# Kernel optimization log

Hardware: AMD Instinct MI355X
Metric: run time of the kernel (lower is better)

## Reference

```python
import jax, jax.numpy as jnp
import numpy as np

G, N, E = 64, 1000, 8192          # graphs, nodes/graph, edges/graph
F_IN, C, H, HID, NCLS = 128, 128, 4, 256, 2
EPS = 1e-5


def _gcn(x, src, dst, W, b):
    # GCNConv: symmetric normalization with self-loops, sum aggregation.
    h = x @ W                                              # [N, C]
    deg = jax.ops.segment_sum(jnp.ones(E, h.dtype), dst, num_segments=N) + 1.0
    dinv = jax.lax.rsqrt(deg)                              # deg^{-1/2}
    msg = h[src] * (dinv[src] * dinv[dst])[:, None]        # [E, C] gather
    out = jax.ops.segment_sum(msg, dst, num_segments=N)    # scatter-add
    out = out + h * (dinv * dinv)[:, None]                 # self-loop term
    return out + b


def _layernorm(y, g, b):
    mu = y.mean(-1, keepdims=True)
    var = ((y - mu) ** 2).mean(-1, keepdims=True)
    return (y - mu) * jax.lax.rsqrt(var + EPS) * g + b


def setup_inputs() -> dict:
    key = jax.random.key(0)
    ks = jax.random.split(key, 12)
    rn = lambda k, s: jax.random.normal(k, s, jnp.float32) * 0.05
    return dict(
        x=jax.random.normal(ks[0], (G, N, F_IN), jnp.float32),
        edge_index=jax.random.randint(ks[1], (G, 2, E), 0, N),
        W0=rn(ks[2], (F_IN, C)), b0=jnp.zeros((C,), jnp.float32),
        W1=rn(ks[3], (C, C)), b1=jnp.zeros((C,), jnp.float32),
        in_w=rn(ks[4], (3 * C, C)), in_b=jnp.zeros((3 * C,), jnp.float32),
        out_w=rn(ks[5], (C, C)), out_b=jnp.zeros((C,), jnp.float32),
        ln2_g=jnp.ones((C,), jnp.float32), ln2_b=jnp.zeros((C,), jnp.float32),
        mw1=rn(ks[6], (C, HID)), mb1=jnp.zeros((HID,), jnp.float32),
        mw2=rn(ks[7], (HID, C)), mb2=jnp.zeros((C,), jnp.float32),
        lw=rn(ks[8], (C, NCLS)), lb=jnp.zeros((NCLS,), jnp.float32),
    )


def reference(x, edge_index, W0, b0, W1, b1, in_w, in_b, out_w, out_b,
              ln2_g, ln2_b, mw1, mb1, mw2, mb2, lw, lb):
    src, dst = edge_index[:, 0, :], edge_index[:, 1, :]
    conv = jax.vmap(_gcn, in_axes=(0, 0, 0, None, None))
    h = jnp.tanh(conv(x, src, dst, W0, b0))   # [G, N, C]
    h = jnp.tanh(conv(h, src, dst, W1, b1))
    g = h.sum(axis=1)                          # SumAggregation -> [G, C]

    # MultiheadAttention, unbatched: sequence of G graph embeddings
    qkv = g @ in_w.T + in_b
    q, k, v = jnp.split(qkv, 3, axis=-1)
    d = C // H
    qh, kh, vh = (t.reshape(G, H, d) for t in (q, k, v))
    attn = jax.nn.softmax(jnp.einsum('qhd,khd->hqk', qh, kh) * (d ** -0.5), axis=-1)
    o = jnp.einsum('hqk,khd->qhd', attn, vh).reshape(G, C) @ out_w.T + out_b

    x_attend = o                               # dropout = identity (eval)
    # NOTE: original computes layer_norm1(x_attend) but immediately overwrites it.
    mlp = jnp.maximum(x_attend @ mw1 + mb1, 0.0) @ mw2 + mb2
    y = _layernorm(x_attend + mlp, ln2_g, ln2_b)
    node_repr = jnp.maximum(y, 0.0).sum(axis=0)  # [C]
    return node_repr @ lw + lb                   # [NCLS]
```

## Files before the change

### kernel.cpp

```cpp
#include <hip/hip_runtime.h>
#include <math.h>

#define Gn 64
#define Nn 1000
#define En 8192
#define Cc 128
#define HIDn 256
#define EPSf 1e-5f

typedef __attribute__((ext_vector_type(8))) short bh8;
typedef __attribute__((ext_vector_type(4))) float fx4;

__device__ __forceinline__ unsigned short f2bf(float f) {
    unsigned u = __float_as_uint(f);
    u += 0x7fffu + ((u >> 16) & 1u);
    return (unsigned short)(u >> 16);
}
__device__ __forceinline__ float bflo(unsigned u) { return __uint_as_float(u << 16); }
__device__ __forceinline__ float bfhi(unsigned u) { return __uint_as_float(u & 0xffff0000u); }

__global__ __launch_bounds__(256) void k_wt(const float* __restrict__ W0, const float* __restrict__ W1,
                                            unsigned short* __restrict__ Wt0g,
                                            unsigned short* __restrict__ Wt1g)
{
    __shared__ __align__(16) short Wls[128][136];
    int t = threadIdx.x;
    const float* Wsrc = (blockIdx.x == 0) ? W0 : W1;
    unsigned short* Wdst = (blockIdx.x == 0) ? Wt0g : Wt1g;
    for (int idx = t; idx < 16384; idx += 256) {
        int kI = idx >> 7, n = idx & 127;
        Wls[n][kI] = (short)f2bf(Wsrc[idx]);
    }
    __syncthreads();
    for (int idx = t; idx < 2048; idx += 256) {
        int n = idx >> 4, kc = idx & 15;
        *(bh8*)(Wdst + (size_t)idx * 8) = *(const bh8*)&Wls[n][kc * 8];
    }
}

__global__ __launch_bounds__(512) void k_front(const int* __restrict__ ei, const float* __restrict__ X,
                                               const unsigned short* __restrict__ Wt0g,
                                               int4* __restrict__ ninfo, int2* __restrict__ epair,
                                               float* __restrict__ pooled, float* __restrict__ repr,
                                               int* __restrict__ bars,
                                               unsigned short* __restrict__ Hout)
{
    __shared__ __align__(16) short Wt[128][136];
    __shared__ int wsum[8];
    int t = threadIdx.x;
    int b = blockIdx.x;

    if (b < 64) {
        int* curs = (int*)&Wt[0][0];
        float* dinv_s = (float*)((char*)&Wt[0][0] + 4096);
        int g = b;
        const int* srcp = ei + (size_t)g * 2 * En;
        const int* dstp = srcp + En;
        int lane = t & 63, wv = t >> 6;

        curs[t * 2] = 0; curs[t * 2 + 1] = 0;
        __syncthreads();
        for (int e = t; e < En; e += 512) atomicAdd(&curs[dstp[e]], 1);
        __syncthreads();

        int base = t * 2;
        int d0 = curs[base], d1 = curs[base + 1];
        int s = d0 + d1;
        int v = s;
        #pragma unroll
        for (int off = 1; off <= 32; off <<= 1) {
            int u = __shfl_up(v, off);
            if (lane >= off) v += u;
        }
        if (lane == 63) wsum[wv] = v;
        __syncthreads();
        int woff = 0;
        #pragma unroll
        for (int w = 0; w < 8; ++w) if (w < wv) woff += wsum[w];
        int e0 = woff + v - s;
        int e1 = e0 + d0;
        float dv0 = rsqrtf((float)d0 + 1.f), dv1 = rsqrtf((float)d1 + 1.f);
        curs[base] = e0; curs[base + 1] = e1;
        dinv_s[base] = dv0; dinv_s[base + 1] = dv1;
        if (base < Nn)     ninfo[g * Nn + base]     = make_int4(e0, d0, __float_as_int(dv0 * dv0), 0);
        if (base + 1 < Nn) ninfo[g * Nn + base + 1] = make_int4(e1, d1, __float_as_int(dv1 * dv1), 0);
        __syncthreads();

        for (int e = t; e < En; e += 512) {
            int dd = dstp[e], ss = srcp[e];
            int p = atomicAdd(&curs[dd], 1);
            float w = dinv_s[ss] * dinv_s[dd];
            epair[(size_t)g * En + p] = make_int2(ss, __float_as_int(w));
        }
        if (t < Cc) pooled[g * Cc + t] = 0.f;
        if (g == 0 && t < Cc) repr[t] = 0.f;
        if (g == 0 && t < 4) bars[t] = 0;
        return;
    }

    int bb = b - 64;
    int xcd = bb & 7, gg = (bb >> 3) & 7, rblk = bb >> 6;
    int g = xcd + 8 * gg;
    for (int idx = t; idx < 2048; idx += 512) {
        int n = idx >> 4, kc = idx & 15;
        *(bh8*)&Wt[n][kc * 8] = *(const bh8*)(Wt0g + (size_t)idx * 8);
    }
    __syncthreads();

    int wave = t >> 6, l = t & 63;
    int lr = l & 15, lg = l >> 4;
    const float* Xf = X + (size_t)g * Nn * Cc;
    unsigned short* Hg = Hout + (size_t)g * Nn * Cc;

    int rbase = rblk * 128 + wave * 16;
    int r = rbase + lr;
    bool ok = r < Nn;
    bh8 af[4];
    #pragma unroll
    for (int ks = 0; ks < 4; ++ks) {
        if (ok) {
            const float* xp = Xf + (size_t)r * Cc + ks * 32 + lg * 8;
            fx4 a0 = *(const fx4*)xp;
            fx4 a1 = *(const fx4*)(xp + 4);
            bh8 av;
            av[0] = (short)f2bf(a0[0]); av[1] = (short)f2bf(a0[1]);
            av[2] = (short)f2bf(a0[2]); av[3] = (short)f2bf(a0[3]);
            av[4] = (short)f2bf(a1[0]); av[5] = (short)f2bf(a1[1]);
            av[6] = (short)f2bf(a1[2]); av[7] = (short)f2bf(a1[3]);
            af[ks] = av;
        } else af[ks] = bh8{0, 0, 0, 0, 0, 0, 0, 0};
    }
    fx4 acc[8];
    #pragma unroll
    for (int ct = 0; ct < 8; ++ct) acc[ct] = fx4{0.f, 0.f, 0.f, 0.f};
    #pragma unroll
    for (int ks = 0; ks < 4; ++ks) {
        #pragma unroll
        for (int ct = 0; ct < 8; ++ct) {
            bh8 bfr = *(const bh8*)(&Wt[ct * 16 + lr][ks * 32 + lg * 8]);
            acc[ct] = __builtin_amdgcn_mfma_f32_16x16x32_bf16(af[ks], bfr, acc[ct], 0, 0, 0);
        }
    }
    #pragma unroll
    for (int ct = 0; ct < 8; ++ct) {
        #pragma unroll
        for (int rg = 0; rg < 4; ++rg) {
            int row = rbase + lg * 4 + rg;
            if (row < Nn) Hg[(size_t)row * Cc + ct * 16 + lr] = f2bf(acc[ct][rg]);
        }
    }
}

__global__ __launch_bounds__(256) void k_gemm1(const unsigned short* __restrict__ Xh,
                                               const unsigned short* __restrict__ Wtg,
                                               unsigned short* __restrict__ Hout)
{
    __shared__ __align__(16) short Wt[128][136];
    int b = blockIdx.x;
    int xcd = b & 7, gg = (b >> 3) & 7, rblk = b >> 6;
    int g = xcd + 8 * gg;
    int t = threadIdx.x;
    for (int idx = t; idx < 2048; idx += 256) {
        int n = idx >> 4, kc = idx & 15;
        bh8 v = *(const bh8*)(Wtg + (size_t)idx * 8);
        *(bh8*)&Wt[n][kc * 8] = v;
    }
    __syncthreads();

    int wave = t >> 6, l = t & 63;
    int lr = l & 15, lg = l >> 4;
    const short* Xg = (const short*)Xh + (size_t)g * Nn * Cc;
    unsigned short* Hg = Hout + (size_t)g * Nn * Cc;

    int rbase = rblk * 64 + wave * 16;
    int r = rbase + lr;
    bool ok = r < Nn;
    bh8 af[4];
    #pragma unroll
    for (int ks = 0; ks < 4; ++ks) {
        if (ok) af[ks] = *(const bh8*)(Xg + (size_t)r * Cc + ks * 32 + lg * 8);
        else    af[ks] = bh8{0, 0, 0, 0, 0, 0, 0, 0};
    }
    fx4 acc[8];
    #pragma unroll
    for (int ct = 0; ct < 8; ++ct) acc[ct] = fx4{0.f, 0.f, 0.f, 0.f};
    #pragma unroll
    for (int ks = 0; ks < 4; ++ks) {
        #pragma unroll
        for (int ct = 0; ct < 8; ++ct) {
            bh8 bfr = *(const bh8*)(&Wt[ct * 16 + lr][ks * 32 + lg * 8]);
            acc[ct] = __builtin_amdgcn_mfma_f32_16x16x32_bf16(af[ks], bfr, acc[ct], 0, 0, 0);
        }
    }
    #pragma unroll
    for (int ct = 0; ct < 8; ++ct) {
        #pragma unroll
        for (int rg = 0; rg < 4; ++rg) {
            int row = rbase + lg * 4 + rg;
            if (row < Nn) Hg[(size_t)row * Cc + ct * 16 + lr] = f2bf(acc[ct][rg]);
        }
    }
}

template<int POOL>
__global__ __launch_bounds__(256) void k_combine(const unsigned* __restrict__ Hb, const int2* __restrict__ epair,
                                                 const int4* __restrict__ ninfo, const float* __restrict__ bias,
                                                 unsigned* __restrict__ Tout, float* __restrict__ pooled)
{
    int b = blockIdx.x;
    int xcd = b & 7, j = b >> 3;
    int g = xcd + 8 * (j & 7);
    int blk = j >> 3;
    int wave = threadIdx.x >> 6, lane = threadIdx.x & 63;
    const unsigned* Hg = Hb + (size_t)g * Nn * 64;
    const int2* epg = epair + (size_t)g * En;
    const int4* nig = ninfo + (size_t)g * Nn;
    float2 bb = *(const float2*)(bias + lane * 2);
    float px = 0.f, py = 0.f;
    for (int n = blk * 4 + wave; n < Nn; n += 128) {
        int4 ni = nig[n];
        int st = ni.x, dc = ni.y;
        float sw = __int_as_float(ni.z);
        unsigned hv = Hg[(size_t)n * 64 + lane];
        float a0x = bflo(hv) * sw + bb.x, a0y = bfhi(hv) * sw + bb.y;
        float a1x = 0.f, a1y = 0.f, a2x = 0.f, a2y = 0.f, a3x = 0.f, a3y = 0.f;
        int e = 0;
        for (; e + 4 <= dc; e += 4) {
            int2 p0 = epg[st + e];
            int2 p1 = epg[st + e + 1];
            int2 p2 = epg[st + e + 2];
            int2 p3 = epg[st + e + 3];
            unsigned r0 = Hg[(size_t)p0.x * 64 + lane];
            unsigned r1 = Hg[(size_t)p1.x * 64 + lane];
            unsigned r2 = Hg[(size_t)p2.x * 64 + lane];
            unsigned r3 = Hg[(size_t)p3.x * 64 + lane];
            float w0 = __int_as_float(p0.y), w1 = __int_as_float(p1.y);
            float w2 = __int_as_float(p2.y), w3 = __int_as_float(p3.y);
            a0x = fmaf(bflo(r0), w0, a0x); a0y = fmaf(bfhi(r0), w0, a0y);
            a1x = fmaf(bflo(r1), w1, a1x); a1y = fmaf(bfhi(r1), w1, a1y);
            a2x = fmaf(bflo(r2), w2, a2x); a2y = fmaf(bfhi(r2), w2, a2y);
            a3x = fmaf(bflo(r3), w3, a3x); a3y = fmaf(bfhi(r3), w3, a3y);
        }
        for (; e < dc; ++e) {
            int2 p0 = epg[st + e];
            unsigned r0 = Hg[(size_t)p0.x * 64 + lane];
            float w0 = __int_as_float(p0.y);
            a0x = fmaf(bflo(r0), w0, a0x); a0y = fmaf(bfhi(r0), w0, a0y);
        }
        float ax = (a0x + a1x) + (a2x + a3x);
        float ay = (a0y + a1y) + (a2y + a3y);
        float tx = tanhf(ax), ty = tanhf(ay);
        if (POOL) { px += tx; py += ty; }
        else Tout[(size_t)(g * Nn + n) * 64 + lane] = ((unsigned)f2bf(ty) << 16) | (unsigned)f2bf(tx);
    }
    if (POOL) {
        atomicAdd(&pooled[g * Cc + lane * 2], px);
        atomicAdd(&pooled[g * Cc + lane * 2 + 1], py);
    }
}

__global__ __launch_bounds__(1024) void k_qkv(const float* __restrict__ pooled, const float* __restrict__ in_w,
                                              const float* __restrict__ in_b, float* __restrict__ qkvb)
{
    int t = threadIdx.x, lane = t & 63, wv = t >> 6;
    int c = blockIdx.x * 16 + wv;
    const float* wr = in_w + c * Cc;
    float w0 = wr[lane], w1 = wr[64 + lane];
    float bias = in_b[c];
    for (int i = 0; i < Gn; ++i) {
        float p = fmaf(pooled[i * Cc + lane], w0, pooled[i * Cc + 64 + lane] * w1);
        #pragma unroll
        for (int off2 = 32; off2 > 0; off2 >>= 1) p += __shfl_xor(p, off2);
        if (lane == 0) qkvb[i * 384 + c] = p + bias;
    }
}

__global__ __launch_bounds__(1024) void k_attn(const float* __restrict__ qkvb, float* __restrict__ ob)
{
    __shared__ float q[64][33], kk[64][33], v[64][33];
    __shared__ float S[64][64];
    int h = blockIdx.x, t = threadIdx.x;

    for (int idx = t; idx < 2048; idx += 1024) {
        int i = idx >> 5, cc = idx & 31;
        q[i][cc]  = qkvb[i * 384 + h * 32 + cc];
        kk[i][cc] = qkvb[i * 384 + 128 + h * 32 + cc];
        v[i][cc]  = qkvb[i * 384 + 256 + h * 32 + cc];
    }
    __syncthreads();

    for (int idx = t; idx < 4096; idx += 1024) {
        int i = idx >> 6, jj = idx & 63;
        float acc = 0.f;
        #pragma unroll
        for (int d2 = 0; d2 < 32; ++d2) acc = fmaf(q[i][d2], kk[jj][d2], acc);
        S[i][jj] = acc * 0.17677669529663687f;
    }
    __syncthreads();

    int lane = t & 63, w = t >> 6;
    for (int r = w; r < 64; r += 16) {
        float val = S[r][lane];
        float m = val;
        #pragma unroll
        for (int off = 32; off > 0; off >>= 1) m = fmaxf(m, __shfl_xor(m, off));
        float e2 = expf(val - m);
        float ssum = e2;
        #pragma unroll
        for (int off = 32; off > 0; off >>= 1) ssum += __shfl_xor(ssum, off);
        S[r][lane] = e2 / ssum;
    }
    __syncthreads();

    for (int idx = t; idx < 2048; idx += 1024) {
        int i = idx >> 5, d2 = idx & 31;
        float acc = 0.f;
        #pragma unroll 4
        for (int k2 = 0; k2 < 64; ++k2) acc = fmaf(S[i][k2], v[k2][d2], acc);
        ob[i * Cc + h * 32 + d2] = acc;
    }
}

__global__ __launch_bounds__(512) void k_tailfinal(const float* __restrict__ ob, const float* __restrict__ out_w,
                                                   const float* __restrict__ out_b, const float* __restrict__ mw1,
                                                   const float* __restrict__ mb1, const float* __restrict__ mw2,
                                                   const float* __restrict__ mb2, const float* __restrict__ ln2g,
                                                   const float* __restrict__ ln2b, const float* __restrict__ lw,
                                                   const float* __restrict__ lb, float* __restrict__ repr,
                                                   int* __restrict__ ctr, float* __restrict__ out)
{
    __shared__ float sob[128];
    __shared__ float sxatt[128];
    __shared__ float sm1p[2][256];
    __shared__ float sm1[256];
    __shared__ float sp2[4][128];
    __shared__ float yb[128];
    __shared__ int slast;
    int g = blockIdx.x;
    int t = threadIdx.x, lane = t & 63, wv = t >> 6;

    if (t < 128) sob[t] = ob[(size_t)g * Cc + t];
    __syncthreads();

    {
        float o0 = sob[lane], o1 = sob[64 + lane];
        for (int c = wv; c < Cc; c += 8) {
            const float* wr = out_w + c * Cc;
            float p = fmaf(o0, wr[lane], o1 * wr[64 + lane]);
            #pragma unroll
            for (int off = 32; off > 0; off >>= 1) p += __shfl_xor(p, off);
            if (lane == 0) sxatt[c] = p + out_b[c];
        }
    }
    __syncthreads();

    {
        int jc = t & 255, half = t >> 8;
        int k0b = half * 64;
        float a[8];
        #pragma unroll
        for (int u = 0; u < 8; ++u) a[u] = 0.f;
        for (int k0 = k0b; k0 < k0b + 64; k0 += 8) {
            #pragma unroll
            for (int u = 0; u < 8; ++u)
                a[u] = fmaf(sxatt[k0 + u], mw1[(size_t)(k0 + u) * HIDn + jc], a[u]);
        }
        sm1p[half][jc] = ((a[0] + a[1]) + (a[2] + a[3])) + ((a[4] + a[5]) + (a[6] + a[7]));
        __syncthreads();
        if (t < 256) sm1[t] = fmaxf(sm1p[0][t] + sm1p[1][t] + mb1[t], 0.f);
    }
    __syncthreads();

    {
        int c = t & 127, q = t >> 7;
        int j0b = q * 64;
        float a[8];
        #pragma unroll
        for (int u = 0; u < 8; ++u) a[u] = 0.f;
        for (int j0 = j0b; j0 < j0b + 64; j0 += 8) {
            #pragma unroll
            for (int u = 0; u < 8; ++u)
                a[u] = fmaf(sm1[j0 + u], mw2[(size_t)(j0 + u) * Cc + c], a[u]);
        }
        sp2[q][c] = ((a[0] + a[1]) + (a[2] + a[3])) + ((a[4] + a[5]) + (a[6] + a[7]));
        __syncthreads();
        if (t < 128) yb[t] = sxatt[t] + (sp2[0][t] + sp2[1][t]) + (sp2[2][t] + sp2[3][t]) + mb2[t];
    }
    __syncthreads();

    if (t < 64) {
        float v0 = yb[lane], v1 = yb[64 + lane];
        float s = v0 + v1;
        #pragma unroll
        for (int off = 32; off > 0; off >>= 1) s += __shfl_xor(s, off);
        float mu = s * (1.f / 128.f);
        float d0 = v0 - mu, d1 = v1 - mu;
        float vv = d0 * d0 + d1 * d1;
        #pragma unroll
        for (int off = 32; off > 0; off >>= 1) vv += __shfl_xor(vv, off);
        float rstd = rsqrtf(vv * (1.f / 128.f) + EPSf);
        float z0 = fmaxf(d0 * rstd * ln2g[lane] + ln2b[lane], 0.f);
        float z1 = fmaxf(d1 * rstd * ln2g[64 + lane] + ln2b[64 + lane], 0.f);
        atomicAdd(&repr[lane], z0);
        atomicAdd(&repr[64 + lane], z1);
    }

    __threadfence();
    __syncthreads();
    if (t == 0) slast = atomicAdd(ctr, 1);
    __syncthreads();
    if (slast == 63) {
        __threadfence();
        __shared__ float r0s[128], r1s[128];
        if (t < 128) {
            float r = __hip_atomic_load(&repr[t], __ATOMIC_RELAXED, __HIP_MEMORY_SCOPE_AGENT);
            r0s[t] = r * lw[t * 2 + 0];
            r1s[t] = r * lw[t * 2 + 1];
        }
        __syncthreads();
        for (int s2 = 64; s2 > 0; s2 >>= 1) {
            if (t < s2) { r0s[t] += r0s[t + s2]; r1s[t] += r1s[t + s2]; }
            __syncthreads();
        }
        if (t == 0) { out[0] = r0s[0] + lb[0]; out[1] = r1s[0] + lb[1]; }
    }
}

extern "C" void kernel_launch(void* const* d_in, const int* in_sizes, int n_in,
                              void* d_out, int out_size, void* d_ws, size_t ws_size,
                              hipStream_t stream)
{
    const float* x     = (const float*)d_in[0];
    const int*   ei    = (const int*)d_in[1];
    const float* W0    = (const float*)d_in[2];
    const float* b0    = (const float*)d_in[3];
    const float* W1    = (const float*)d_in[4];
    const float* b1    = (const float*)d_in[5];
    const float* in_w  = (const float*)d_in[6];
    const float* in_b  = (const float*)d_in[7];
    const float* out_w = (const float*)d_in[8];
    const float* out_b = (const float*)d_in[9];
    const float* ln2g  = (const float*)d_in[10];
    const float* ln2b  = (const float*)d_in[11];
    const float* mw1   = (const float*)d_in[12];
    const float* mb1   = (const float*)d_in[13];
    const float* mw2   = (const float*)d_in[14];
    const float* mb2   = (const float*)d_in[15];
    const float* lw    = (const float*)d_in[16];
    const float* lb    = (const float*)d_in[17];
    float* out = (float*)d_out;
    (void)in_sizes; (void)n_in; (void)out_size; (void)ws_size;

    char* ws = (char*)d_ws;
    size_t off = 0;
    auto carve = [&](size_t bytes) { size_t o = off; off += (bytes + 255) & ~(size_t)255; return o; };
    size_t o_ni    = carve((size_t)Gn * Nn * 16);
    size_t o_ep    = carve((size_t)Gn * En * 8);
    size_t o_pool  = carve((size_t)Gn * Cc * 4);
    size_t o_qkv   = carve((size_t)Gn * 384 * 4);
    size_t o_ob    = carve((size_t)Gn * Cc * 4);
    size_t o_repr  = carve((size_t)Cc * 4);
    size_t o_bars  = carve(256);
    size_t o_W0t   = carve((size_t)Cc * Cc * 2);
    size_t o_W1t   = carve((size_t)Cc * Cc * 2);
    size_t o_H     = carve((size_t)Gn * Nn * Cc * 2);
    size_t o_T     = carve((size_t)Gn * Nn * Cc * 2);

    int4*  ninfo  = (int4*)(ws + o_ni);
    int2*  epair  = (int2*)(ws + o_ep);
    float* pooled = (float*)(ws + o_pool);
    float* qkvb   = (float*)(ws + o_qkv);
    float* ob     = (float*)(ws + o_ob);
    float* repr   = (float*)(ws + o_repr);
    int*   bars   = (int*)(ws + o_bars);
    unsigned short* Wt0g = (unsigned short*)(ws + o_W0t);
    unsigned short* Wt1g = (unsigned short*)(ws + o_W1t);
    unsigned short* H  = (unsigned short*)(ws + o_H);
    unsigned short* T  = (unsigned short*)(ws + o_T);

    k_wt<<<2, 256, 0, stream>>>(W0, W1, Wt0g, Wt1g);
    k_front<<<576, 512, 0, stream>>>(ei, x, Wt0g, ninfo, epair, pooled, repr, bars, H);
    k_combine<0><<<2048, 256, 0, stream>>>((const unsigned*)H, epair, ninfo, b0, (unsigned*)T, nullptr);
    k_gemm1<<<1024, 256, 0, stream>>>(T, Wt1g, H);
    k_combine<1><<<2048, 256, 0, stream>>>((const unsigned*)H, epair, ninfo, b1, nullptr, pooled);
    k_qkv<<<24, 1024, 0, stream>>>(pooled, in_w, in_b, qkvb);
    k_attn<<<4, 1024, 0, stream>>>(qkvb, ob);
    k_tailfinal<<<64, 512, 0, stream>>>(ob, out_w, out_b, mw1, mb1, mw2, mb2, ln2g, ln2b,
                                        lw, lb, repr, &bars[2], out);
}
```

Measured before the change: 160.1 us.

## Fuse attention into tail kernel, use fast tanh and pre-scaled gather offsets

Removes the separate 4-block attention kernel. Each tail block now recomputes its own query row's attention over all keys and values loaded into shared memory, which saves one launch and the round trip through the ob buffer. Separately, the combine kernels use an exp2/rcp based tanh instead of tanhf and store edge source indices pre-shifted to byte offsets, which removes multiply/size_t address arithmetic in the gather loop. The trade-off is that every tail block redundantly loads all 64 K/V rows (about 66KB of shared memory), and the fast tanh has slightly different accuracy.

Result: faster. 152.0 us (median of 2 runs) (-5.1%).

```diff
diff --git a/kernel.cpp b/kernel.cpp
--- a/kernel.cpp
+++ b/kernel.cpp
@@ -18,6 +18,10 @@
 }
 __device__ __forceinline__ float bflo(unsigned u) { return __uint_as_float(u << 16); }
 __device__ __forceinline__ float bfhi(unsigned u) { return __uint_as_float(u & 0xffff0000u); }
+__device__ __forceinline__ float tanh_fast(float x) {
+    float e = exp2f(x * 2.885390081777927f);
+    return 1.f - 2.f * __builtin_amdgcn_rcpf(e + 1.f);
+}
 
 __global__ __launch_bounds__(256) void k_wt(const float* __restrict__ W0, const float* __restrict__ W1,
                                             unsigned short* __restrict__ Wt0g,
@@ -90,7 +94,7 @@
             int dd = dstp[e], ss = srcp[e];
             int p = atomicAdd(&curs[dd], 1);
             float w = dinv_s[ss] * dinv_s[dd];
-            epair[(size_t)g * En + p] = make_int2(ss, __float_as_int(w));
+            epair[(size_t)g * En + p] = make_int2(ss << 8, __float_as_int(w));
         }
         if (t < Cc) pooled[g * Cc + t] = 0.f;
         if (g == 0 && t < Cc) repr[t] = 0.f;
@@ -212,16 +216,17 @@
     int g = xcd + 8 * (j & 7);
     int blk = j >> 3;
     int wave = threadIdx.x >> 6, lane = threadIdx.x & 63;
-    const unsigned* Hg = Hb + (size_t)g * Nn * 64;
+    const char* Hgc = (const char*)(Hb + (size_t)g * Nn * 64);
     const int2* epg = epair + (size_t)g * En;
     const int4* nig = ninfo + (size_t)g * Nn;
     float2 bb = *(const float2*)(bias + lane * 2);
+    int lb4 = lane * 4;
     float px = 0.f, py = 0.f;
     for (int n = blk * 4 + wave; n < Nn; n += 128) {
         int4 ni = nig[n];
         int st = ni.x, dc = ni.y;
         float sw = __int_as_float(ni.z);
-        unsigned hv = Hg[(size_t)n * 64 + lane];
+        unsigned hv = *(const unsigned*)(Hgc + n * 256 + lb4);
         float a0x = bflo(hv) * sw + bb.x, a0y = bfhi(hv) * sw + bb.y;
         float a1x = 0.f, a1y = 0.f, a2x = 0.f, a2y = 0.f, a3x = 0.f, a3y = 0.f;
         int e = 0;
@@ -230,10 +235,10 @@
             int2 p1 = epg[st + e + 1];
             int2 p2 = epg[st + e + 2];
             int2 p3 = epg[st + e + 3];
-            unsigned r0 = Hg[(size_t)p0.x * 64 + lane];
-            unsigned r1 = Hg[(size_t)p1.x * 64 + lane];
-            unsigned r2 = Hg[(size_t)p2.x * 64 + lane];
-            unsigned r3 = Hg[(size_t)p3.x * 64 + lane];
+            unsigned r0 = *(const unsigned*)(Hgc + p0.x + lb4);
+            unsigned r1 = *(const unsigned*)(Hgc + p1.x + lb4);
+            unsigned r2 = *(const unsigned*)(Hgc + p2.x + lb4);
+            unsigned r3 = *(const unsigned*)(Hgc + p3.x + lb4);
             float w0 = __int_as_float(p0.y), w1 = __int_as_float(p1.y);
             float w2 = __int_as_float(p2.y), w3 = __int_as_float(p3.y);
             a0x = fmaf(bflo(r0), w0, a0x); a0y = fmaf(bfhi(r0), w0, a0y);
@@ -243,13 +248,13 @@
         }
         for (; e < dc; ++e) {
             int2 p0 = epg[st + e];
-            unsigned r0 = Hg[(size_t)p0.x * 64 + lane];
+            unsigned r0 = *(const unsigned*)(Hgc + p0.x + lb4);
             float w0 = __int_as_float(p0.y);
             a0x = fmaf(bflo(r0), w0, a0x); a0y = fmaf(bfhi(r0), w0, a0y);
         }
         float ax = (a0x + a1x) + (a2x + a3x);
         float ay = (a0y + a1y) + (a2y + a3y);
-        float tx = tanhf(ax), ty = tanhf(ay);
+        float tx = tanh_fast(ax), ty = tanh_fast(ay);
         if (POOL) { px += tx; py += ty; }
         else Tout[(size_t)(g * Nn + n) * 64 + lane] = ((unsigned)f2bf(ty) << 16) | (unsigned)f2bf(tx);
     }
@@ -275,60 +280,18 @@
     }
 }
 
-__global__ __launch_bounds__(1024) void k_attn(const float* __restrict__ qkvb, float* __restrict__ ob)
-{
-    __shared__ float q[64][33], kk[64][33], v[64][33];
-    __shared__ float S[64][64];
-    int h = blockIdx.x, t = threadIdx.x;
-
-    for (int idx = t; idx < 2048; idx += 1024) {
-        int i = idx >> 5, cc = idx & 31;
-        q[i][cc]  = qkvb[i * 384 + h * 32 + cc];
-        kk[i][cc] = qkvb[i * 384 + 128 + h * 32 + cc];
-        v[i][cc]  = qkvb[i * 384 + 256 + h * 32 + cc];
-    }
-    __syncthreads();
-
-    for (int idx = t; idx < 4096; idx += 1024) {
-        int i = idx >> 6, jj = idx & 63;
-        float acc = 0.f;
-        #pragma unroll
-        for (int d2 = 0; d2 < 32; ++d2) acc = fmaf(q[i][d2], kk[jj][d2], acc);
-        S[i][jj] = acc * 0.17677669529663687f;
-    }
-    __syncthreads();
-
-    int lane = t & 63, w = t >> 6;
-    for (int r = w; r < 64; r += 16) {
-        float val = S[r][lane];
-        float m = val;
-        #pragma unroll
-        for (int off = 32; off > 0; off >>= 1) m = fmaxf(m, __shfl_xor(m, off));
-        float e2 = expf(val - m);
-        float ssum = e2;
-        #pragma unroll
-        for (int off = 32; off > 0; off >>= 1) ssum += __shfl_xor(ssum, off);
-        S[r][lane] = e2 / ssum;
-    }
-    __syncthreads();
-
-    for (int idx = t; idx < 2048; idx += 1024) {
-        int i = idx >> 5, d2 = idx & 31;
-        float acc = 0.f;
-        #pragma unroll 4
-        for (int k2 = 0; k2 < 64; ++k2) acc = fmaf(S[i][k2], v[k2][d2], acc);
-        ob[i * Cc + h * 32 + d2] = acc;
-    }
-}
-
-__global__ __launch_bounds__(512) void k_tailfinal(const float* __restrict__ ob, const float* __restrict__ out_w,
-                                                   const float* __restrict__ out_b, const float* __restrict__ mw1,
-                                                   const float* __restrict__ mb1, const float* __restrict__ mw2,
-                                                   const float* __restrict__ mb2, const float* __restrict__ ln2g,
-                                                   const float* __restrict__ ln2b, const float* __restrict__ lw,
-                                                   const float* __restrict__ lb, float* __restrict__ repr,
-                                                   int* __restrict__ ctr, float* __restrict__ out)
-{
+__global__ __launch_bounds__(512) void k_tail(const float* __restrict__ qkvb, const float* __restrict__ out_w,
+                                              const float* __restrict__ out_b, const float* __restrict__ mw1,
+                                              const float* __restrict__ mb1, const float* __restrict__ mw2,
+                                              const float* __restrict__ mb2, const float* __restrict__ ln2g,
+                                              const float* __restrict__ ln2b, const float* __restrict__ lw,
+                                              const float* __restrict__ lb, float* __restrict__ repr,
+                                              int* __restrict__ ctr, float* __restrict__ out)
+{
+    __shared__ float kk[64][129];
+    __shared__ float vv[64][129];
+    __shared__ float qrow[128];
+    __shared__ float S[4][64];
     __shared__ float sob[128];
     __shared__ float sxatt[128];
     __shared__ float sm1p[2][256];
@@ -339,7 +302,43 @@
     int g = blockIdx.x;
     int t = threadIdx.x, lane = t & 63, wv = t >> 6;
 
-    if (t < 128) sob[t] = ob[(size_t)g * Cc + t];
+    for (int idx = t; idx < 8192; idx += 512) {
+        int i = idx >> 7, c = idx & 127;
+        kk[i][c] = qkvb[i * 384 + 128 + c];
+        vv[i][c] = qkvb[i * 384 + 256 + c];
+    }
+    if (t < 128) qrow[t] = qkvb[g * 384 + t];
+    __syncthreads();
+
+    if (t < 256) {
+        int h = t >> 6, jj = t & 63;
+        int base = h * 32;
+        float acc = 0.f;
+        #pragma unroll
+        for (int d = 0; d < 32; ++d) acc = fmaf(qrow[base + d], kk[jj][base + d], acc);
+        S[h][jj] = acc * 0.17677669529663687f;
+    }
+    __syncthreads();
+    if (wv < 4) {
+        float val = S[wv][lane];
+        float m = val;
+        #pragma unroll
+        for (int off = 32; off > 0; off >>= 1) m = fmaxf(m, __shfl_xor(m, off));
+        float e2 = expf(val - m);
+        float ssum = e2;
+        #pragma unroll
+        for (int off = 32; off > 0; off >>= 1) ssum += __shfl_xor(ssum, off);
+        S[wv][lane] = e2 / ssum;
+    }
+    __syncthreads();
+    if (t < 128) {
+        int h = t >> 5, d = t & 31;
+        int col = h * 32 + d;
+        float acc = 0.f;
+        #pragma unroll 4
+        for (int j = 0; j < 64; ++j) acc = fmaf(S[h][j], vv[j][col], acc);
+        sob[col] = acc;
+    }
     __syncthreads();
 
     {
@@ -395,10 +394,10 @@
         for (int off = 32; off > 0; off >>= 1) s += __shfl_xor(s, off);
         float mu = s * (1.f / 128.f);
         float d0 = v0 - mu, d1 = v1 - mu;
-        float vv = d0 * d0 + d1 * d1;
-        #pragma unroll
-        for (int off = 32; off > 0; off >>= 1) vv += __shfl_xor(vv, off);
-        float rstd = rsqrtf(vv * (1.f / 128.f) + EPSf);
+        float vvr = d0 * d0 + d1 * d1;
+        #pragma unroll
+        for (int off = 32; off > 0; off >>= 1) vvr += __shfl_xor(vvr, off);
+        float rstd = rsqrtf(vvr * (1.f / 128.f) + EPSf);
         float z0 = fmaxf(d0 * rstd * ln2g[lane] + ln2b[lane], 0.f);
         float z1 = fmaxf(d1 * rstd * ln2g[64 + lane] + ln2b[64 + lane], 0.f);
         atomicAdd(&repr[lane], z0);
@@ -458,7 +457,6 @@
     size_t o_ep    = carve((size_t)Gn * En * 8);
     size_t o_pool  = carve((size_t)Gn * Cc * 4);
     size_t o_qkv   = carve((size_t)Gn * 384 * 4);
-    size_t o_ob    = carve((size_t)Gn * Cc * 4);
     size_t o_repr  = carve((size_t)Cc * 4);
     size_t o_bars  = carve(256);
     size_t o_W0t   = carve((size_t)Cc * Cc * 2);
@@ -470,7 +468,6 @@
     int2*  epair  = (int2*)(ws + o_ep);
     float* pooled = (float*)(ws + o_pool);
     float* qkvb   = (float*)(ws + o_qkv);
-    float* ob     = (float*)(ws + o_ob);
     float* repr   = (float*)(ws + o_repr);
     int*   bars   = (int*)(ws + o_bars);
     unsigned short* Wt0g = (unsigned short*)(ws + o_W0t);
@@ -484,7 +481,6 @@
     k_gemm1<<<1024, 256, 0, stream>>>(T, Wt1g, H);
     k_combine<1><<<2048, 256, 0, stream>>>((const unsigned*)H, epair, ninfo, b1, nullptr, pooled);
     k_qkv<<<24, 1024, 0, stream>>>(pooled, in_w, in_b, qkvb);
-    k_attn<<<4, 1024, 0, stream>>>(qkvb, ob);
-    k_tailfinal<<<64, 512, 0, stream>>>(ob, out_w, out_b, mw1, mb1, mw2, mb2, ln2g, ln2b,
-                                        lw, lb, repr, &bars[2], out);
-}
+    k_tail<<<64, 512, 0, stream>>>(qkvb, out_w, out_b, mw1, mb1, mw2, mb2, ln2g, ln2b,
+                                   lw, lb, repr, &bars[2], out);
+}
```
